# Kernel tuning notes

Measured on AMD Instinct MI355X. Metric: run time of the kernel, lower is better.

## Reference

```python
import jax, jax.numpy as jnp
import numpy as np

N = 100000      # nodes
E = 1600000     # edges (avg degree 16)
DIN = 128
DOUT = 128


def setup_inputs() -> dict:
    key = jax.random.key(0)
    k1, k2, k3, k4 = jax.random.split(key, 4)
    x = jax.random.normal(k1, (N, DIN), dtype=jnp.float32)
    edge_index = jax.random.randint(k2, (2, E), 0, N, dtype=jnp.int64)
    # guarantee every node appears at least once as a source row so that
    # degree > 0 everywhere (1/sqrt(0) would be inf, as in the torch code)
    row = edge_index[0].at[:N].set(jnp.arange(N, dtype=jnp.int64))
    edge_index = jnp.stack([row, edge_index[1]])
    W = jax.random.normal(k3, (DOUT, DIN), dtype=jnp.float32) / np.sqrt(DIN)
    b = jax.random.normal(k4, (DOUT,), dtype=jnp.float32) * 0.01
    return {"x": x, "edge_index": edge_index, "W": W, "b": b}


def reference(x, edge_index, W, b):
    # Math identical to: A = dense(add_self_loops(edge_index));
    # D = 1/sqrt(degree(edge_index[0]))  (degree WITHOUT self-loops);
    # out = (D_i * A_ij * D_j) @ (x W^T + b)
    row, col = edge_index[0], edge_index[1]
    deg = jax.ops.segment_sum(jnp.ones(row.shape[0], x.dtype), row, num_segments=N)
    d = jax.lax.rsqrt(deg)                      # [N]
    h = x @ W.T + b                             # [N, DOUT]
    # edge contributions: out[r] += D[r] * D[c] * h[c]  (duplicate edges sum, as to_dense does)
    agg = jax.ops.segment_sum(d[col][:, None] * h[col], row, num_segments=N)
    # self-loop term added for every node: D[i]^2 * h[i]
    out = d[:, None] * agg + (d * d)[:, None] * h
    return out
```

## Files before the change

kernel.cpp:

```cpp
#include <hip/hip_runtime.h>

#define D 128
#define BROWS 512
#define LOGB 9
#define NBMAX 256
#define CAP 9216
#define CHUNK 4096
#define LDSW 136

typedef __attribute__((ext_vector_type(8))) short bf16x8;
typedef __attribute__((ext_vector_type(4))) float f32x4;

__device__ inline unsigned short f2bf(float f) {
    unsigned u = __float_as_uint(f);
    u += 0x7FFFu + ((u >> 16) & 1u);
    return (unsigned short)(u >> 16);
}
__device__ inline float bf2f(unsigned short h) {
    return __uint_as_float((unsigned)h << 16);
}
__device__ inline float bflo(unsigned u) { return __uint_as_float(u << 16); }
__device__ inline float bfhi(unsigned u) { return __uint_as_float(u & 0xFFFF0000u); }

__global__ __launch_bounds__(512) void k_bin(const int* __restrict__ row,
                                             const int* __restrict__ col,
                                             int E, int* __restrict__ gcur,
                                             unsigned* __restrict__ ebuf,
                                             const float* __restrict__ W,
                                             unsigned short* __restrict__ Wbh,
                                             unsigned short* __restrict__ Wbl) {
    __shared__ int lhist[NBMAX];
    __shared__ int sc[NBMAX];
    __shared__ int gbase[NBMAX];
    __shared__ unsigned sstage[CHUNK];
    __shared__ int sdest[CHUNK];
    int t = threadIdx.x;
    if (blockIdx.x < 8) {
        int base = blockIdx.x * 2048 + t;
        #pragma unroll
        for (int i = 0; i < 4; ++i) {
            int idx = base + i * 512;
            float wv = W[idx];
            unsigned short h = f2bf(wv);
            Wbh[idx] = h;
            Wbl[idx] = f2bf(wv - bf2f(h));
        }
    }
    int base = blockIdx.x * CHUNK;
    if (t < NBMAX) lhist[t] = 0;
    __syncthreads();
    int b[8], p[8]; unsigned pk[8];
    #pragma unroll
    for (int i = 0; i < 8; ++i) {
        int idx = base + i * 512 + t;
        if (idx < E) {
            int r = row[idx], c = col[idx];
            b[i] = r >> LOGB;
            pk[i] = ((unsigned)(r & (BROWS - 1)) << 17) | (unsigned)c;
            p[i] = atomicAdd(&lhist[b[i]], 1);
        } else b[i] = -1;
    }
    __syncthreads();
    if (t < 64) {
        int a0 = lhist[4*t], a1 = lhist[4*t+1], a2 = lhist[4*t+2], a3 = lhist[4*t+3];
        int s = a0 + a1 + a2 + a3;
        int incl = s;
        #pragma unroll
        for (int m = 1; m < 64; m <<= 1) {
            int tmp = __shfl_up(incl, m);
            if (t >= m) incl += tmp;
        }
        int excl = incl - s;
        sc[4*t] = excl; sc[4*t+1] = excl + a0;
        sc[4*t+2] = excl + a0 + a1; sc[4*t+3] = excl + a0 + a1 + a2;
        if (a0 > 0) gbase[4*t]   = atomicAdd(&gcur[4*t],   a0);
        if (a1 > 0) gbase[4*t+1] = atomicAdd(&gcur[4*t+1], a1);
        if (a2 > 0) gbase[4*t+2] = atomicAdd(&gcur[4*t+2], a2);
        if (a3 > 0) gbase[4*t+3] = atomicAdd(&gcur[4*t+3], a3);
    }
    __syncthreads();
    #pragma unroll
    for (int i = 0; i < 8; ++i) {
        if (b[i] >= 0) {
            int lidx = sc[b[i]] + p[i];
            int rel = gbase[b[i]] + p[i];
            sstage[lidx] = pk[i];
            sdest[lidx] = (rel < CAP) ? (b[i] * CAP + rel) : -1;
        }
    }
    __syncthreads();
    int total = sc[NBMAX - 1] + lhist[NBMAX - 1];
    for (int i = t; i < total; i += 512) {
        int d = sdest[i];
        if (d >= 0) ebuf[d] = sstage[i];
    }
}

__global__ __launch_bounds__(1024) void k_group(const int* __restrict__ gcur,
                                                const unsigned* __restrict__ ebuf,
                                                int N, int NBK,
                                                float* __restrict__ dvals,
                                                int* __restrict__ rptr,
                                                int* __restrict__ csr_col,
                                                unsigned short* __restrict__ Hs) {
    __shared__ unsigned sebuf[CAP];
    __shared__ int lhist[BROWS];
    __shared__ int wtot[8];
    __shared__ int woff[8];
    __shared__ int sebase;
    int bkt = blockIdx.x, t = threadIdx.x;
    int cnt = gcur[bkt]; if (cnt > CAP) cnt = CAP;
    if (t < 64) {
        int acc = 0;
        for (int i = t; i < bkt; i += 64) {
            int g = gcur[i];
            acc += (g > CAP) ? CAP : g;
        }
        #pragma unroll
        for (int m = 1; m < 64; m <<= 1) acc += __shfl_xor(acc, m);
        if (t == 0) sebase = acc;
    }
    if (t < BROWS) lhist[t] = 0;
    __syncthreads();
    const unsigned* ep = ebuf + (size_t)bkt * CAP;
    for (int i = t; i < cnt; i += 1024) {
        unsigned e = ep[i];
        sebuf[i] = e;
        atomicAdd(&lhist[e >> 17], 1);
    }
    __syncthreads();
    int lane = t & 63, wv = t >> 6;
    int v = 0, incl = 0;
    if (t < BROWS) {
        v = lhist[t];
        incl = v;
        #pragma unroll
        for (int m = 1; m < 64; m <<= 1) {
            int tmp = __shfl_up(incl, m);
            if (lane >= m) incl += tmp;
        }
        if (lane == 63) wtot[wv] = incl;
    }
    __syncthreads();
    if (t < 8) {
        int w = wtot[t];
        int wincl = w;
        #pragma unroll
        for (int m = 1; m < 8; m <<= 1) {
            int tmp = __shfl_up(wincl, m);
            if (t >= m) wincl += tmp;
        }
        woff[t] = wincl - w;
    }
    __syncthreads();
    int ebase = sebase;
    if (t < BROWS) {
        int excl = woff[wv] + incl - v;
        int r = (bkt << LOGB) + t;
        if (r < N) {
            rptr[r] = ebase + excl;
            dvals[r] = rsqrtf((float)v);
        }
        lhist[t] = excl;
    }
    if (bkt == NBK - 1 && t == 0) rptr[N] = ebase + cnt;
    if (bkt == 0 && t == 0) dvals[N] = 0.f;
    if (bkt == 0 && t < 64)
        ((unsigned*)(Hs + (size_t)N * D))[t] = 0u;
    __syncthreads();
    for (int i = t; i < cnt; i += 1024) {
        unsigned e = sebuf[i];
        int rr = (int)(e >> 17);
        int p = atomicAdd(&lhist[rr], 1);
        csr_col[ebase + p] = (int)(e & 0x1FFFFu);
    }
}

__global__ __launch_bounds__(256, 2) void k_gc(const float* __restrict__ x,
                                               const unsigned short* __restrict__ Wbh,
                                               const unsigned short* __restrict__ Wbl,
                                               const float* __restrict__ b,
                                               const float* __restrict__ dvals,
                                               unsigned short* __restrict__ Hs, int N) {
    __shared__ unsigned short Whi[128 * LDSW];
    __shared__ unsigned short Wlo[128 * LDSW];
    __shared__ float bs[D];
    int t = threadIdx.x;
    #pragma unroll
    for (int i = 0; i < 16; ++i) {
        int idx4 = i * 256 + t;
        int r = idx4 >> 5;
        int c = (idx4 & 31) * 4;
        ((ushort4*)&Whi[r * LDSW + c])[0] = ((const ushort4*)Wbh)[idx4];
        ((ushort4*)&Wlo[r * LDSW + c])[0] = ((const ushort4*)Wbl)[idx4];
    }
    if (t < D) bs[t] = b[t];
    __syncthreads();

    int wave = t >> 6, lane = t & 63;
    int quad = lane >> 4, mrow = lane & 15;
    int row_base = blockIdx.x * 128 + wave * 32;

    bf16x8 Ahi[2][4], Alo[2][4];
    #pragma unroll
    for (int s = 0; s < 2; ++s) {
        int grow = row_base + s * 16 + mrow;
        bool ok = grow < N;
        const float* xrow = x + (size_t)(ok ? grow : 0) * D;
        #pragma unroll
        for (int kk = 0; kk < 4; ++kk) {
            int k0 = kk * 32 + quad * 8;
            float4 f0 = ok ? ((const float4*)(xrow + k0))[0] : make_float4(0, 0, 0, 0);
            float4 f1 = ok ? ((const float4*)(xrow + k0))[1] : make_float4(0, 0, 0, 0);
            float fv[8] = {f0.x, f0.y, f0.z, f0.w, f1.x, f1.y, f1.z, f1.w};
            #pragma unroll
            for (int j = 0; j < 8; ++j) {
                unsigned short h = f2bf(fv[j]);
                Ahi[s][kk][j] = (short)h;
                Alo[s][kk][j] = (short)f2bf(fv[j] - bf2f(h));
            }
        }
    }

    f32x4 acc[2][8];
    #pragma unroll
    for (int s = 0; s < 2; ++s)
        #pragma unroll
        for (int ct = 0; ct < 8; ++ct)
            acc[s][ct] = (f32x4){0.f, 0.f, 0.f, 0.f};

    #pragma unroll
    for (int ct = 0; ct < 8; ++ct) {
        int wrow = ct * 16 + mrow;
        #pragma unroll
        for (int kk = 0; kk < 4; ++kk) {
            int off = wrow * LDSW + kk * 32 + quad * 8;
            bf16x8 Bhi = *(const bf16x8*)&Whi[off];
            bf16x8 Blo = *(const bf16x8*)&Wlo[off];
            #pragma unroll
            for (int s = 0; s < 2; ++s) {
                acc[s][ct] = __builtin_amdgcn_mfma_f32_16x16x32_bf16(Ahi[s][kk], Bhi, acc[s][ct], 0, 0, 0);
                acc[s][ct] = __builtin_amdgcn_mfma_f32_16x16x32_bf16(Alo[s][kk], Bhi, acc[s][ct], 0, 0, 0);
                acc[s][ct] = __builtin_amdgcn_mfma_f32_16x16x32_bf16(Ahi[s][kk], Blo, acc[s][ct], 0, 0, 0);
            }
        }
    }

    __syncthreads();
    unsigned short* stage = Whi;
    #pragma unroll
    for (int s = 0; s < 2; ++s) {
        #pragma unroll
        for (int r = 0; r < 4; ++r) {
            int grow = row_base + s * 16 + quad * 4 + r;
            float dv = dvals[(grow < N) ? grow : N];
            int lrow = wave * 32 + s * 16 + quad * 4 + r;
            #pragma unroll
            for (int ct = 0; ct < 8; ++ct) {
                int col = ct * 16 + mrow;
                stage[lrow * LDSW + col] = f2bf(dv * (acc[s][ct][r] + bs[col]));
            }
        }
    }
    __syncthreads();
    for (int i = t; i < 128 * 16; i += 256) {
        int lrow = i >> 4;
        int g = i & 15;
        int grow = blockIdx.x * 128 + lrow;
        if (grow < N)
            ((uint4*)Hs)[(size_t)grow * 16 + g] =
                ((const uint4*)&stage[lrow * LDSW])[g];
    }
}

#define ACC8(v) do { \
    a[0] += bflo((v).x); a[1] += bfhi((v).x); \
    a[2] += bflo((v).y); a[3] += bfhi((v).y); \
    a[4] += bflo((v).z); a[5] += bfhi((v).z); \
    a[6] += bflo((v).w); a[7] += bfhi((v).w); } while (0)

__global__ __launch_bounds__(256) void k_rows(const unsigned short* __restrict__ Hs,
                                              const int* __restrict__ rptr,
                                              const int* __restrict__ csr_col,
                                              const float* __restrict__ dvals,
                                              float* __restrict__ out, int N) {
    int wid = (blockIdx.x * blockDim.x + threadIdx.x) >> 6;
    if (wid >= N) return;
    int lane = threadIdx.x & 63;
    int grp = lane >> 4, sl = lane & 15;
    int s = rptr[wid];
    int n = rptr[wid + 1] - s;
    const uint4* hv = (const uint4*)Hs;

    int cc = csr_col[s + lane];
    int ccreg = (lane < n) ? cc : N;
    uint4 vself = hv[(size_t)wid * 16 + sl];

    float a[8] = {0.f, 0.f, 0.f, 0.f, 0.f, 0.f, 0.f, 0.f};
    int nf = (n < 64) ? n : 64;

    int c0 = __shfl(ccreg, grp);
    int c1 = __shfl(ccreg, grp + 4);
    int c2 = __shfl(ccreg, grp + 8);
    int c3 = __shfl(ccreg, grp + 12);
    uint4 p0 = hv[(size_t)c0 * 16 + sl];
    uint4 p1 = hv[(size_t)c1 * 16 + sl];
    uint4 p2 = hv[(size_t)c2 * 16 + sl];
    uint4 p3 = hv[(size_t)c3 * 16 + sl];

    for (int k0 = 16; k0 < nf; k0 += 16) {
        int i0 = k0 + grp;
        int d0 = __shfl(ccreg, i0);
        int d1 = __shfl(ccreg, i0 + 4);
        int d2 = __shfl(ccreg, i0 + 8);
        int d3 = __shfl(ccreg, i0 + 12);
        uint4 q0 = hv[(size_t)d0 * 16 + sl];
        uint4 q1 = hv[(size_t)d1 * 16 + sl];
        uint4 q2 = hv[(size_t)d2 * 16 + sl];
        uint4 q3 = hv[(size_t)d3 * 16 + sl];
        ACC8(p0); ACC8(p1); ACC8(p2); ACC8(p3);
        p0 = q0; p1 = q1; p2 = q2; p3 = q3;
    }
    ACC8(p0); ACC8(p1); ACC8(p2); ACC8(p3);

    if (__builtin_expect(n > 64, 0)) {
        for (int idx = 64 + grp; idx < n; idx += 4) {
            int c = csr_col[s + idx];
            uint4 v = hv[(size_t)c * 16 + sl];
            ACC8(v);
        }
    }
    if (grp == 0) ACC8(vself);

    #pragma unroll
    for (int j = 0; j < 8; ++j) {
        a[j] += __shfl_xor(a[j], 16);
        a[j] += __shfl_xor(a[j], 32);
    }
    float dr = dvals[wid];
    if (grp < 2) {
        float4 o = (grp == 0) ? make_float4(a[0], a[1], a[2], a[3])
                              : make_float4(a[4], a[5], a[6], a[7]);
        o.x *= dr; o.y *= dr; o.z *= dr; o.w *= dr;
        ((float4*)(out + (size_t)wid * D))[sl * 2 + grp] = o;
    }
}

extern "C" void kernel_launch(void* const* d_in, const int* in_sizes, int n_in,
                              void* d_out, int out_size, void* d_ws, size_t ws_size,
                              hipStream_t stream) {
    const float* x  = (const float*)d_in[0];
    const int*   ei = (const int*)d_in[1];
    const float* W  = (const float*)d_in[2];
    const float* b  = (const float*)d_in[3];
    float* out = (float*)d_out;
    int N = in_sizes[0] / D;
    int E = in_sizes[1] / 2;
    int NB = (N + BROWS - 1) / BROWS;
    int NCH = (E + CHUNK - 1) / CHUNK;

    int*            gcur    = (int*)d_ws;
    int*            rptr    = gcur + NBMAX;
    float*          dvals   = (float*)(rptr + N + 1);
    int*            csr_col = (int*)(dvals + N + 1);
    unsigned*       ebuf    = (unsigned*)(csr_col + E + 64);
    unsigned short* Wbh     = (unsigned short*)(ebuf + (size_t)NB * CAP);
    unsigned short* Wbl     = Wbh + D * D;
    uintptr_t hs_addr = (uintptr_t)(Wbl + D * D);
    hs_addr = (hs_addr + 15) & ~(uintptr_t)15;
    unsigned short* Hs = (unsigned short*)hs_addr;

    hipMemsetAsync(gcur, 0, NBMAX * sizeof(int), stream);
    k_bin<<<NCH, 512, 0, stream>>>(ei, ei + E, E, gcur, ebuf, W, Wbh, Wbl);
    k_group<<<NB, 1024, 0, stream>>>(gcur, ebuf, N, NB, dvals, rptr, csr_col, Hs);
    k_gc<<<(N + 127) / 128, 256, 0, stream>>>(x, Wbh, Wbl, b, dvals, Hs, N);
    k_rows<<<(N + 3) / 4, 256, 0, stream>>>(Hs, rptr, csr_col, dvals, out, N);
}
```

Baseline: 252.4 us.

## Replace atomic global bucket scatter with per-chunk sorted writes and gather

The binning kernel no longer reserves space in global per-bucket buffers with atomics. Each chunk now writes its locally bucket-sorted edges contiguously and saves its per-bucket prefix offsets, and the grouping kernel gathers each bucket's segments from every chunk. This removes the memset, the global atomics and the scattered writes, making the k_bin stores coalesced. In exchange, k_group reads many small segments (about 391 chunks per bucket) and computes its global base with a shared atomic sum over chunk offsets.

```diff
diff --git a/kernel.cpp b/kernel.cpp
--- a/kernel.cpp
+++ b/kernel.cpp
@@ -4,8 +4,9 @@
 #define BROWS 512
 #define LOGB 9
 #define NBMAX 256
-#define CAP 9216
 #define CHUNK 4096
+#define SCAP 10240
+#define NCHMAX 512
 #define LDSW 136
 
 typedef __attribute__((ext_vector_type(8))) short bf16x8;
@@ -24,22 +25,20 @@
 
 __global__ __launch_bounds__(512) void k_bin(const int* __restrict__ row,
                                              const int* __restrict__ col,
-                                             int E, int* __restrict__ gcur,
-                                             unsigned* __restrict__ ebuf,
+                                             int E, unsigned* __restrict__ ebuf,
+                                             int* __restrict__ sc_g,
                                              const float* __restrict__ W,
                                              unsigned short* __restrict__ Wbh,
                                              unsigned short* __restrict__ Wbl) {
     __shared__ int lhist[NBMAX];
     __shared__ int sc[NBMAX];
-    __shared__ int gbase[NBMAX];
     __shared__ unsigned sstage[CHUNK];
-    __shared__ int sdest[CHUNK];
     int t = threadIdx.x;
     if (blockIdx.x < 8) {
-        int base = blockIdx.x * 2048 + t;
+        int wb = blockIdx.x * 2048 + t;
         #pragma unroll
         for (int i = 0; i < 4; ++i) {
-            int idx = base + i * 512;
+            int idx = wb + i * 512;
             float wv = W[idx];
             unsigned short h = f2bf(wv);
             Wbh[idx] = h;
@@ -73,73 +72,93 @@
         int excl = incl - s;
         sc[4*t] = excl; sc[4*t+1] = excl + a0;
         sc[4*t+2] = excl + a0 + a1; sc[4*t+3] = excl + a0 + a1 + a2;
-        if (a0 > 0) gbase[4*t]   = atomicAdd(&gcur[4*t],   a0);
-        if (a1 > 0) gbase[4*t+1] = atomicAdd(&gcur[4*t+1], a1);
-        if (a2 > 0) gbase[4*t+2] = atomicAdd(&gcur[4*t+2], a2);
-        if (a3 > 0) gbase[4*t+3] = atomicAdd(&gcur[4*t+3], a3);
-    }
-    __syncthreads();
-    #pragma unroll
-    for (int i = 0; i < 8; ++i) {
-        if (b[i] >= 0) {
-            int lidx = sc[b[i]] + p[i];
-            int rel = gbase[b[i]] + p[i];
-            sstage[lidx] = pk[i];
-            sdest[lidx] = (rel < CAP) ? (b[i] * CAP + rel) : -1;
-        }
     }
     __syncthreads();
     int total = sc[NBMAX - 1] + lhist[NBMAX - 1];
-    for (int i = t; i < total; i += 512) {
-        int d = sdest[i];
-        if (d >= 0) ebuf[d] = sstage[i];
-    }
-}
-
-__global__ __launch_bounds__(1024) void k_group(const int* __restrict__ gcur,
+    #pragma unroll
+    for (int i = 0; i < 8; ++i)
+        if (b[i] >= 0) sstage[sc[b[i]] + p[i]] = pk[i];
+    if (t < 257) sc_g[blockIdx.x * 257 + t] = (t < 256) ? sc[t] : total;
+    __syncthreads();
+    for (int i = t; i < total; i += 512)
+        ebuf[base + i] = sstage[i];
+}
+
+__global__ __launch_bounds__(1024) void k_group(const int* __restrict__ sc_g,
                                                 const unsigned* __restrict__ ebuf,
-                                                int N, int NBK,
+                                                int N, int NBK, int NCH,
                                                 float* __restrict__ dvals,
                                                 int* __restrict__ rptr,
                                                 int* __restrict__ csr_col,
                                                 unsigned short* __restrict__ Hs) {
-    __shared__ unsigned sebuf[CAP];
+    __shared__ unsigned sebuf[SCAP];
     __shared__ int lhist[BROWS];
-    __shared__ int wtot[8];
-    __shared__ int woff[8];
-    __shared__ int sebase;
+    __shared__ int chS[NCHMAX], chO[NCHMAX], chL[NCHMAX];
+    __shared__ int wtot[16], woff[16];
+    __shared__ int sEbase, sCnt;
     int bkt = blockIdx.x, t = threadIdx.x;
-    int cnt = gcur[bkt]; if (cnt > CAP) cnt = CAP;
-    if (t < 64) {
-        int acc = 0;
-        for (int i = t; i < bkt; i += 64) {
-            int g = gcur[i];
-            acc += (g > CAP) ? CAP : g;
-        }
-        #pragma unroll
-        for (int m = 1; m < 64; m <<= 1) acc += __shfl_xor(acc, m);
-        if (t == 0) sebase = acc;
-    }
+    int lane = t & 63, wv = t >> 6;
+
+    int s0 = 0, len = 0;
+    if (t < NCH) {
+        s0 = sc_g[t * 257 + bkt];
+        len = sc_g[t * 257 + bkt + 1] - s0;
+    }
+    if (t == 0) sEbase = 0;
     if (t < BROWS) lhist[t] = 0;
     __syncthreads();
-    const unsigned* ep = ebuf + (size_t)bkt * CAP;
-    for (int i = t; i < cnt; i += 1024) {
-        unsigned e = ep[i];
-        sebuf[i] = e;
-        atomicAdd(&lhist[e >> 17], 1);
-    }
-    __syncthreads();
-    int lane = t & 63, wv = t >> 6;
-    int v = 0, incl = 0;
+    if (t < NCH) { chS[t] = s0; atomicAdd(&sEbase, s0); }
+    int incl = len;
+    #pragma unroll
+    for (int m = 1; m < 64; m <<= 1) {
+        int tmp = __shfl_up(incl, m);
+        if (lane >= m) incl += tmp;
+    }
+    if (lane == 63) wtot[wv] = incl;
+    __syncthreads();
+    if (t < 16) {
+        int w = wtot[t];
+        int wincl = w;
+        #pragma unroll
+        for (int m = 1; m < 16; m <<= 1) {
+            int tmp = __shfl_up(wincl, m);
+            if (t >= m) wincl += tmp;
+        }
+        woff[t] = wincl - w;
+        if (t == 15) sCnt = wincl;
+    }
+    __syncthreads();
+    if (t < NCH) {
+        int off = woff[wv] + incl - len;
+        int l = len;
+        if (off > SCAP) off = SCAP;
+        if (off + l > SCAP) l = SCAP - off;
+        chO[t] = off;
+        chL[t] = l;
+    }
+    __syncthreads();
+    for (int ch = wv; ch < NCH; ch += 16) {
+        int so = chS[ch], off = chO[ch], l = chL[ch];
+        for (int b0 = 0; b0 < l; b0 += 64) {
+            int k = b0 + lane;
+            if (k < l) sebuf[off + k] = ebuf[(size_t)ch * CHUNK + so + k];
+        }
+    }
+    __syncthreads();
+    int cnt = sCnt; if (cnt > SCAP) cnt = SCAP;
+    for (int i = t; i < cnt; i += 1024)
+        atomicAdd(&lhist[sebuf[i] >> 17], 1);
+    __syncthreads();
+    int v = 0, incl2 = 0;
     if (t < BROWS) {
         v = lhist[t];
-        incl = v;
+        incl2 = v;
         #pragma unroll
         for (int m = 1; m < 64; m <<= 1) {
-            int tmp = __shfl_up(incl, m);
-            if (lane >= m) incl += tmp;
-        }
-        if (lane == 63) wtot[wv] = incl;
+            int tmp = __shfl_up(incl2, m);
+            if (lane >= m) incl2 += tmp;
+        }
+        if (lane == 63) wtot[wv] = incl2;
     }
     __syncthreads();
     if (t < 8) {
@@ -153,9 +172,9 @@
         woff[t] = wincl - w;
     }
     __syncthreads();
-    int ebase = sebase;
+    int ebase = sEbase;
     if (t < BROWS) {
-        int excl = woff[wv] + incl - v;
+        int excl = woff[wv] + incl2 - v;
         int r = (bkt << LOGB) + t;
         if (r < N) {
             rptr[r] = ebase + excl;
@@ -359,20 +378,19 @@
     int NB = (N + BROWS - 1) / BROWS;
     int NCH = (E + CHUNK - 1) / CHUNK;
 
-    int*            gcur    = (int*)d_ws;
-    int*            rptr    = gcur + NBMAX;
+    int*            rptr    = (int*)d_ws;
     float*          dvals   = (float*)(rptr + N + 1);
     int*            csr_col = (int*)(dvals + N + 1);
     unsigned*       ebuf    = (unsigned*)(csr_col + E + 64);
-    unsigned short* Wbh     = (unsigned short*)(ebuf + (size_t)NB * CAP);
+    int*            sc_g    = (int*)(ebuf + (size_t)NCH * CHUNK);
+    unsigned short* Wbh     = (unsigned short*)(sc_g + (size_t)NCH * 257);
     unsigned short* Wbl     = Wbh + D * D;
     uintptr_t hs_addr = (uintptr_t)(Wbl + D * D);
     hs_addr = (hs_addr + 15) & ~(uintptr_t)15;
     unsigned short* Hs = (unsigned short*)hs_addr;
 
-    hipMemsetAsync(gcur, 0, NBMAX * sizeof(int), stream);
-    k_bin<<<NCH, 512, 0, stream>>>(ei, ei + E, E, gcur, ebuf, W, Wbh, Wbl);
-    k_group<<<NB, 1024, 0, stream>>>(gcur, ebuf, N, NB, dvals, rptr, csr_col, Hs);
+    k_bin<<<NCH, 512, 0, stream>>>(ei, ei + E, E, ebuf, sc_g, W, Wbh, Wbl);
+    k_group<<<NB, 1024, 0, stream>>>(sc_g, ebuf, N, NB, NCH, dvals, rptr, csr_col, Hs);
     k_gc<<<(N + 127) / 128, 256, 0, stream>>>(x, Wbh, Wbl, b, dvals, Hs, N);
     k_rows<<<(N + 3) / 4, 256, 0, stream>>>(Hs, rptr, csr_col, dvals, out, N);
 }
```

After: 236.8 us. -6.2%, faster.
